# Optimization experiments

Hardware: AMD Instinct MI355X
Metric: run time of the kernel (lower is better)

Reference implementation:

```python
import jax, jax.numpy as jnp
import numpy as np

B, IN, H = 64, 1024, 1024

def _lin(x, W, b):
    # torch nn.Linear: y = x @ W.T + b, W:[out,in]
    return x @ W.T + b

def setup_inputs() -> dict:
    key = jax.random.key(0)
    ks = jax.random.split(key, 16)
    s_in = 1.0 / np.sqrt(IN)
    s_cat = 1.0 / np.sqrt(IN + H)
    s_h = 1.0 / np.sqrt(H)
    return {
        "x": jax.random.normal(ks[0], (B, IN), jnp.float32),
        "h": jax.random.normal(ks[1], (B, H), jnp.float32),
        "C": jax.random.normal(ks[2], (B, H, H), jnp.float32) * 0.02,
        "Wq": jax.random.normal(ks[3], (H, IN), jnp.float32) * s_in,
        "bq": jax.random.normal(ks[4], (H,), jnp.float32) * s_in,
        "Wk": jax.random.normal(ks[5], (H, IN), jnp.float32) * s_in,
        "bk": jax.random.normal(ks[6], (H,), jnp.float32) * s_in,
        "Wv": jax.random.normal(ks[7], (H, IN), jnp.float32) * s_in,
        "bv": jax.random.normal(ks[8], (H,), jnp.float32) * s_in,
        "Wf": jax.random.normal(ks[9], (H, IN + H), jnp.float32) * s_cat,
        "bf": jax.random.normal(ks[10], (H,), jnp.float32) * s_cat,
        "Wi": jax.random.normal(ks[11], (H, IN + H), jnp.float32) * s_cat,
        "bi": jax.random.normal(ks[12], (H,), jnp.float32) * s_cat,
        "Wo": jax.random.normal(ks[13], (H, H), jnp.float32) * s_h,
        "bo": jax.random.normal(ks[14], (H,), jnp.float32) * s_h,
    }

def reference(x, h, C, Wq, bq, Wk, bk, Wv, bv, Wf, bf, Wi, bi, Wo, bo):
    q = _lin(x, Wq, bq)            # [B,H]
    k = _lin(x, Wk, bk)            # [B,H]
    v = _lin(x, Wv, bv)            # [B,H]
    combined = jnp.concatenate([x, h], axis=-1)       # [B,IN+H]
    f = jax.nn.sigmoid(_lin(combined, Wf, bf))        # [B,H]
    i = jax.nn.sigmoid(_lin(combined, Wi, bi))        # [B,H]
    # gated matrix-memory update: C_new[b,m,n] = f[b,m]*C[b,m,n] + i[b,m]*k[b,m]*v[b,n]
    C_new = f[:, :, None] * C + (i * k)[:, :, None] * v[:, None, :]
    # readout: matvec with q then tanh and output projection
    r = jnp.einsum('bmn,bn->bm', C_new, q)            # [B,H]
    h_new = _lin(jnp.tanh(r), Wo, bo)                 # [B,H]
    return (h_new, C_new)
```

## Files before the change

### kernel.cpp

```cpp
#include <hip/hip_runtime.h>
#include <math.h>

#define HB 64
#define HD 1024
#define KS 128
#define XS 68

typedef float f32x4 __attribute__((ext_vector_type(4)));

__device__ __forceinline__ void splitk_tile(
    const float* __restrict__ X0, int noff,
    const float* __restrict__ W, int K,
    int m0, int k0,
    float* __restrict__ P)
{
    __shared__ __align__(16) float Xs[32][XS];
    __shared__ __align__(16) float Ws[32][XS];
    const int t  = threadIdx.x;
    const int bx = t & 15;
    const int my = t >> 4;
    float acc[4][4] = {};

    for (int kc = 0; kc < KS; kc += 32) {
        const int n0 = k0 + kc;
        #pragma unroll
        for (int i = 0; i < 2; ++i) {
            int u = t + 256 * i;
            int b = u >> 3, nq = u & 7;
            float4 xv = *(const float4*)&X0[b * HD + (n0 - noff) + nq * 4];
            Xs[nq * 4 + 0][b] = xv.x; Xs[nq * 4 + 1][b] = xv.y;
            Xs[nq * 4 + 2][b] = xv.z; Xs[nq * 4 + 3][b] = xv.w;
        }
        #pragma unroll
        for (int i = 0; i < 2; ++i) {
            int u = t + 256 * i;
            int mm = u >> 3, nq = u & 7;
            float4 wv = *(const float4*)&W[(long long)(m0 + mm) * K + n0 + nq * 4];
            Ws[nq * 4 + 0][mm] = wv.x; Ws[nq * 4 + 1][mm] = wv.y;
            Ws[nq * 4 + 2][mm] = wv.z; Ws[nq * 4 + 3][mm] = wv.w;
        }
        __syncthreads();
        #pragma unroll
        for (int n = 0; n < 32; ++n) {
            float4 xv = *(const float4*)&Xs[n][bx * 4];
            float4 wv = *(const float4*)&Ws[n][my * 4];
            float xe[4] = {xv.x, xv.y, xv.z, xv.w};
            float we[4] = {wv.x, wv.y, wv.z, wv.w};
            #pragma unroll
            for (int i = 0; i < 4; ++i)
                #pragma unroll
                for (int j = 0; j < 4; ++j)
                    acc[i][j] = fmaf(xe[i], we[j], acc[i][j]);
        }
        __syncthreads();
    }
    #pragma unroll
    for (int i = 0; i < 4; ++i)
        #pragma unroll
        for (int j = 0; j < 4; ++j)
            P[(bx * 4 + i) * HD + m0 + my * 4 + j] = acc[i][j];
}

__global__ __launch_bounds__(256) void qkvfi_splitk(
    const float* __restrict__ x, const float* __restrict__ h,
    const float* __restrict__ Wq, const float* __restrict__ Wk,
    const float* __restrict__ Wv, const float* __restrict__ Wf,
    const float* __restrict__ Wi, float* __restrict__ P)
{
    const int gy = blockIdx.y;
    const float* W; int K, split;
    if (gy < 24) {
        int g = gy >> 3; split = gy & 7; K = HD;
        W = (g == 0) ? Wq : (g == 1) ? Wk : Wv;
    } else {
        int tt = gy - 24; int g = tt >> 4; split = tt & 15; K = 2 * HD;
        W = g ? Wi : Wf;
    }
    const int k0 = split * KS;
    const float* X0; int noff;
    if (k0 < HD) { X0 = x; noff = 0; } else { X0 = h; noff = HD; }
    splitk_tile(X0, noff, W, K, blockIdx.x * 64, k0, P + (size_t)gy * (HB * HD));
}

__global__ __launch_bounds__(256) void out_splitk(
    const float* __restrict__ tr, const float* __restrict__ Wo,
    float* __restrict__ P2)
{
    const int split = blockIdx.y;
    splitk_tile(tr, 0, Wo, HD, blockIdx.x * 64, split * KS,
                P2 + (size_t)split * (HB * HD));
}

__global__ __launch_bounds__(256) void reduce_qkvfi(
    const float* __restrict__ P,
    const float* __restrict__ bq, const float* __restrict__ bk,
    const float* __restrict__ bv, const float* __restrict__ bfv,
    const float* __restrict__ biv,
    float* __restrict__ q, float* __restrict__ k, float* __restrict__ v,
    float* __restrict__ fg, float* __restrict__ ig)
{
    const int o = blockIdx.x * 256 + threadIdx.x;
    const int g = o >> 16;
    const int rem = o & 65535;
    const int m = rem & (HD - 1);
    int base, ns, act; const float* bias; float* out;
    switch (g) {
        case 0:  base = 0;  ns = 8;  bias = bq;  out = q;  act = 0; break;
        case 1:  base = 8;  ns = 8;  bias = bk;  out = k;  act = 0; break;
        case 2:  base = 16; ns = 8;  bias = bv;  out = v;  act = 0; break;
        case 3:  base = 24; ns = 16; bias = bfv; out = fg; act = 1; break;
        default: base = 40; ns = 16; bias = biv; out = ig; act = 1; break;
    }
    float s = bias[m];
    for (int i = 0; i < ns; ++i) s += P[(size_t)(base + i) * 65536 + rem];
    if (act) s = 1.0f / (1.0f + expf(-s));
    out[rem] = s;
}

__global__ __launch_bounds__(256) void reduce_out(
    const float* __restrict__ P2, const float* __restrict__ bo,
    float* __restrict__ hnew)
{
    const int o = blockIdx.x * 256 + threadIdx.x;
    const int m = o & (HD - 1);
    float s = bo[m];
    #pragma unroll
    for (int i = 0; i < 8; ++i) s += P2[(size_t)i * 65536 + o];
    hnew[o] = s;
}

__global__ __launch_bounds__(256) void update_kernel(
    const float* __restrict__ C,
    const float* __restrict__ q, const float* __restrict__ k,
    const float* __restrict__ v, const float* __restrict__ fg,
    const float* __restrict__ ig,
    float* __restrict__ Cn, float* __restrict__ tr)
{
    const int wid  = threadIdx.x >> 6;
    const int lane = threadIdx.x & 63;
    const int row  = blockIdx.x * 4 + wid;
    const int b    = row >> 10;
    const int m    = row & (HD - 1);

    const float fm  = fg[b * HD + m];
    const float ikm = ig[b * HD + m] * k[b * HD + m];

    const f32x4* C4 = (const f32x4*)C;
    const float4* V4 = (const float4*)v;
    const float4* Q4 = (const float4*)q;
    f32x4*       N4 = (f32x4*)Cn;

    const int base  = row * (HD / 4);
    const int vbase = b * (HD / 4);

    float racc = 0.f;
    #pragma unroll
    for (int j = 0; j < 4; ++j) {
        int o = lane + 64 * j;
        f32x4 c4 = __builtin_nontemporal_load(&C4[base + o]);
        float4 v4 = V4[vbase + o];
        float4 q4 = Q4[vbase + o];
        f32x4 cn;
        cn.x = fmaf(fm, c4.x, ikm * v4.x);
        cn.y = fmaf(fm, c4.y, ikm * v4.y);
        cn.z = fmaf(fm, c4.z, ikm * v4.z);
        cn.w = fmaf(fm, c4.w, ikm * v4.w);
        __builtin_nontemporal_store(cn, &N4[base + o]);
        racc += cn.x * q4.x + cn.y * q4.y + cn.z * q4.z + cn.w * q4.w;
    }
    #pragma unroll
    for (int off = 32; off; off >>= 1) racc += __shfl_xor(racc, off);
    if (lane == 0) tr[row] = tanhf(racc);
}

extern "C" void kernel_launch(void* const* d_in, const int* in_sizes, int n_in,
                              void* d_out, int out_size, void* d_ws, size_t ws_size,
                              hipStream_t stream) {
    const float* x  = (const float*)d_in[0];
    const float* h  = (const float*)d_in[1];
    const float* C  = (const float*)d_in[2];
    const float* Wq = (const float*)d_in[3];
    const float* bq = (const float*)d_in[4];
    const float* Wk = (const float*)d_in[5];
    const float* bk = (const float*)d_in[6];
    const float* Wv = (const float*)d_in[7];
    const float* bv = (const float*)d_in[8];
    const float* Wf = (const float*)d_in[9];
    const float* bf = (const float*)d_in[10];
    const float* Wi = (const float*)d_in[11];
    const float* bi = (const float*)d_in[12];
    const float* Wo = (const float*)d_in[13];
    const float* bo = (const float*)d_in[14];

    float* outp = (float*)d_out;
    float* hnew = outp;
    float* Cn   = outp + HB * HD;

    const size_t SL = (size_t)HB * HD;
    float* ws = (float*)d_ws;
    float* q  = ws + 0 * SL;
    float* k  = ws + 1 * SL;
    float* v  = ws + 2 * SL;
    float* fg = ws + 3 * SL;
    float* ig = ws + 4 * SL;
    float* tr = ws + 5 * SL;
    float* P  = ws + 6 * SL;
    float* P2 = ws + 62 * SL;

    qkvfi_splitk<<<dim3(16, 56), 256, 0, stream>>>(x, h, Wq, Wk, Wv, Wf, Wi, P);
    reduce_qkvfi<<<dim3(1280), 256, 0, stream>>>(P, bq, bk, bv, bf, bi,
                                                 q, k, v, fg, ig);
    update_kernel<<<dim3((HB * HD) / 4), 256, 0, stream>>>(
        C, q, k, v, fg, ig, Cn, tr);
    out_splitk<<<dim3(16, 8), 256, 0, stream>>>(tr, Wo, P2);
    reduce_out<<<dim3(256), 256, 0, stream>>>(P2, bo, hnew);
}
```

Before: 128.7 us.

## Use split-bf16 MFMA for projection GEMMs and vectorize reductions

Replaces the shared-memory FP32 SIMT split-K tiles with bf16 MFMA 16x16x32 instructions. Operands are split into hi and lo bf16 parts and three MFMAs per fragment approximate FP32 accuracy. Fragments are loaded directly from global memory without LDS staging or barriers. The reduce kernels now process float4 per thread with fewer blocks. This trades FP32 exactness for near-FP32 accuracy, and each block re-loads and converts its operands.

```diff
diff --git a/kernel.cpp b/kernel.cpp
--- a/kernel.cpp
+++ b/kernel.cpp
@@ -4,64 +4,69 @@
 #define HB 64
 #define HD 1024
 #define KS 128
-#define XS 68
-
-typedef float f32x4 __attribute__((ext_vector_type(4)));
-
-__device__ __forceinline__ void splitk_tile(
+
+typedef float f32x4  __attribute__((ext_vector_type(4)));
+typedef short bf16x8 __attribute__((ext_vector_type(8)));
+
+__device__ __forceinline__ unsigned short f2bf(float f) {
+    unsigned int u = __float_as_uint(f);
+    u += 0x7fffu + ((u >> 16) & 1u);
+    return (unsigned short)(u >> 16);
+}
+__device__ __forceinline__ float bf2f(unsigned short h) {
+    unsigned int u = ((unsigned int)h) << 16;
+    return __uint_as_float(u);
+}
+
+__device__ __forceinline__ void ldfrag2(const float* __restrict__ p,
+                                        bf16x8& hi, bf16x8& lo) {
+    float4 a = *(const float4*)p;
+    float4 b = *(const float4*)(p + 4);
+    float e[8] = {a.x, a.y, a.z, a.w, b.x, b.y, b.z, b.w};
+    #pragma unroll
+    for (int i = 0; i < 8; ++i) {
+        unsigned short h = f2bf(e[i]);
+        hi[i] = (short)h;
+        lo[i] = (short)f2bf(e[i] - bf2f(h));
+    }
+}
+
+__device__ __forceinline__ void mfma_tile(
     const float* __restrict__ X0, int noff,
     const float* __restrict__ W, int K,
     int m0, int k0,
     float* __restrict__ P)
 {
-    __shared__ __align__(16) float Xs[32][XS];
-    __shared__ __align__(16) float Ws[32][XS];
-    const int t  = threadIdx.x;
-    const int bx = t & 15;
-    const int my = t >> 4;
-    float acc[4][4] = {};
-
-    for (int kc = 0; kc < KS; kc += 32) {
-        const int n0 = k0 + kc;
+    const int t     = threadIdx.x;
+    const int w     = t >> 6;
+    const int l     = t & 63;
+    const int row16 = l & 15;
+    const int g     = l >> 4;
+    const int mbase = m0 + w * 16;
+
+    f32x4 acc[4] = {};
+    #pragma unroll
+    for (int kk = 0; kk < 4; ++kk) {
+        const int kabs = k0 + kk * 32 + g * 8;
+        bf16x8 wh, wl;
+        ldfrag2(&W[(long long)(mbase + row16) * K + kabs], wh, wl);
         #pragma unroll
-        for (int i = 0; i < 2; ++i) {
-            int u = t + 256 * i;
-            int b = u >> 3, nq = u & 7;
-            float4 xv = *(const float4*)&X0[b * HD + (n0 - noff) + nq * 4];
-            Xs[nq * 4 + 0][b] = xv.x; Xs[nq * 4 + 1][b] = xv.y;
-            Xs[nq * 4 + 2][b] = xv.z; Xs[nq * 4 + 3][b] = xv.w;
+        for (int bs = 0; bs < 4; ++bs) {
+            bf16x8 xh, xl;
+            ldfrag2(&X0[(bs * 16 + row16) * HD + kabs - noff], xh, xl);
+            acc[bs] = __builtin_amdgcn_mfma_f32_16x16x32_bf16(xh, wh, acc[bs], 0, 0, 0);
+            acc[bs] = __builtin_amdgcn_mfma_f32_16x16x32_bf16(xh, wl, acc[bs], 0, 0, 0);
+            acc[bs] = __builtin_amdgcn_mfma_f32_16x16x32_bf16(xl, wh, acc[bs], 0, 0, 0);
         }
+    }
+    #pragma unroll
+    for (int bs = 0; bs < 4; ++bs)
         #pragma unroll
-        for (int i = 0; i < 2; ++i) {
-            int u = t + 256 * i;
-            int mm = u >> 3, nq = u & 7;
-            float4 wv = *(const float4*)&W[(long long)(m0 + mm) * K + n0 + nq * 4];
-            Ws[nq * 4 + 0][mm] = wv.x; Ws[nq * 4 + 1][mm] = wv.y;
-            Ws[nq * 4 + 2][mm] = wv.z; Ws[nq * 4 + 3][mm] = wv.w;
-        }
-        __syncthreads();
-        #pragma unroll
-        for (int n = 0; n < 32; ++n) {
-            float4 xv = *(const float4*)&Xs[n][bx * 4];
-            float4 wv = *(const float4*)&Ws[n][my * 4];
-            float xe[4] = {xv.x, xv.y, xv.z, xv.w};
-            float we[4] = {wv.x, wv.y, wv.z, wv.w};
-            #pragma unroll
-            for (int i = 0; i < 4; ++i)
-                #pragma unroll
-                for (int j = 0; j < 4; ++j)
-                    acc[i][j] = fmaf(xe[i], we[j], acc[i][j]);
-        }
-        __syncthreads();
-    }
-    #pragma unroll
-    for (int i = 0; i < 4; ++i)
-        #pragma unroll
-        for (int j = 0; j < 4; ++j)
-            P[(bx * 4 + i) * HD + m0 + my * 4 + j] = acc[i][j];
-}
-
-__global__ __launch_bounds__(256) void qkvfi_splitk(
+        for (int r = 0; r < 4; ++r)
+            P[(bs * 16 + g * 4 + r) * HD + mbase + row16] = acc[bs][r];
+}
+
+__global__ __launch_bounds__(256) void qkvfi_mfma(
     const float* __restrict__ x, const float* __restrict__ h,
     const float* __restrict__ Wq, const float* __restrict__ Wk,
     const float* __restrict__ Wv, const float* __restrict__ Wf,
@@ -79,16 +84,16 @@
     const int k0 = split * KS;
     const float* X0; int noff;
     if (k0 < HD) { X0 = x; noff = 0; } else { X0 = h; noff = HD; }
-    splitk_tile(X0, noff, W, K, blockIdx.x * 64, k0, P + (size_t)gy * (HB * HD));
-}
-
-__global__ __launch_bounds__(256) void out_splitk(
+    mfma_tile(X0, noff, W, K, blockIdx.x * 64, k0, P + (size_t)gy * (HB * HD));
+}
+
+__global__ __launch_bounds__(256) void out_mfma(
     const float* __restrict__ tr, const float* __restrict__ Wo,
     float* __restrict__ P2)
 {
     const int split = blockIdx.y;
-    splitk_tile(tr, 0, Wo, HD, blockIdx.x * 64, split * KS,
-                P2 + (size_t)split * (HB * HD));
+    mfma_tile(tr, 0, Wo, HD, blockIdx.x * 64, split * KS,
+              P2 + (size_t)split * (HB * HD));
 }
 
 __global__ __launch_bounds__(256) void reduce_qkvfi(
@@ -99,10 +104,10 @@
     float* __restrict__ q, float* __restrict__ k, float* __restrict__ v,
     float* __restrict__ fg, float* __restrict__ ig)
 {
-    const int o = blockIdx.x * 256 + threadIdx.x;
-    const int g = o >> 16;
-    const int rem = o & 65535;
-    const int m = rem & (HD - 1);
+    const int o4 = blockIdx.x * 256 + threadIdx.x;
+    const int g  = o4 >> 14;
+    const int r4 = o4 & 16383;
+    const int m4 = r4 & 255;
     int base, ns, act; const float* bias; float* out;
     switch (g) {
         case 0:  base = 0;  ns = 8;  bias = bq;  out = q;  act = 0; break;
@@ -111,22 +116,33 @@
         case 3:  base = 24; ns = 16; bias = bfv; out = fg; act = 1; break;
         default: base = 40; ns = 16; bias = biv; out = ig; act = 1; break;
     }
-    float s = bias[m];
-    for (int i = 0; i < ns; ++i) s += P[(size_t)(base + i) * 65536 + rem];
-    if (act) s = 1.0f / (1.0f + expf(-s));
-    out[rem] = s;
+    float4 s = ((const float4*)bias)[m4];
+    const float4* P4 = (const float4*)P;
+    for (int i = 0; i < ns; ++i) {
+        float4 p = P4[(size_t)(base + i) * 16384 + r4];
+        s.x += p.x; s.y += p.y; s.z += p.z; s.w += p.w;
+    }
+    if (act) {
+        s.x = 1.0f / (1.0f + expf(-s.x)); s.y = 1.0f / (1.0f + expf(-s.y));
+        s.z = 1.0f / (1.0f + expf(-s.z)); s.w = 1.0f / (1.0f + expf(-s.w));
+    }
+    ((float4*)out)[r4] = s;
 }
 
 __global__ __launch_bounds__(256) void reduce_out(
     const float* __restrict__ P2, const float* __restrict__ bo,
     float* __restrict__ hnew)
 {
-    const int o = blockIdx.x * 256 + threadIdx.x;
-    const int m = o & (HD - 1);
-    float s = bo[m];
-    #pragma unroll
-    for (int i = 0; i < 8; ++i) s += P2[(size_t)i * 65536 + o];
-    hnew[o] = s;
+    const int o4 = blockIdx.x * 256 + threadIdx.x;
+    const int m4 = o4 & 255;
+    float4 s = ((const float4*)bo)[m4];
+    const float4* P4 = (const float4*)P2;
+    #pragma unroll
+    for (int i = 0; i < 8; ++i) {
+        float4 p = P4[(size_t)i * 16384 + o4];
+        s.x += p.x; s.y += p.y; s.z += p.z; s.w += p.w;
+    }
+    ((float4*)hnew)[o4] = s;
 }
 
 __global__ __launch_bounds__(256) void update_kernel(
@@ -145,10 +161,10 @@
     const float fm  = fg[b * HD + m];
     const float ikm = ig[b * HD + m] * k[b * HD + m];
 
-    const f32x4* C4 = (const f32x4*)C;
+    const f32x4*  C4 = (const f32x4*)C;
     const float4* V4 = (const float4*)v;
     const float4* Q4 = (const float4*)q;
-    f32x4*       N4 = (f32x4*)Cn;
+    f32x4*        N4 = (f32x4*)Cn;
 
     const int base  = row * (HD / 4);
     const int vbase = b * (HD / 4);
@@ -207,11 +223,11 @@
     float* P  = ws + 6 * SL;
     float* P2 = ws + 62 * SL;
 
-    qkvfi_splitk<<<dim3(16, 56), 256, 0, stream>>>(x, h, Wq, Wk, Wv, Wf, Wi, P);
-    reduce_qkvfi<<<dim3(1280), 256, 0, stream>>>(P, bq, bk, bv, bf, bi,
-                                                 q, k, v, fg, ig);
+    qkvfi_mfma<<<dim3(16, 56), 256, 0, stream>>>(x, h, Wq, Wk, Wv, Wf, Wi, P);
+    reduce_qkvfi<<<dim3(320), 256, 0, stream>>>(P, bq, bk, bv, bf, bi,
+                                                q, k, v, fg, ig);
     update_kernel<<<dim3((HB * HD) / 4), 256, 0, stream>>>(
         C, q, k, v, fg, ig, Cn, tr);
-    out_splitk<<<dim3(16, 8), 256, 0, stream>>>(tr, Wo, P2);
-    reduce_out<<<dim3(256), 256, 0, stream>>>(P2, bo, hnew);
-}
+    out_mfma<<<dim3(16, 8), 256, 0, stream>>>(tr, Wo, P2);
+    reduce_out<<<dim3(64), 256, 0, stream>>>(P2, bo, hnew);
+}
```

Measured after the change: 136.0 us. 1.06x slower.
